# Kernel optimization log

Hardware: AMD Instinct MI355X
Metric: run time of the kernel (lower is better)

## Reference

```python
import jax, jax.numpy as jnp
import numpy as np

RC, RMIN = 6.0, 0.5
BETA, M1, M2 = 12, 24, 6
B, N, NT, MN = 4, 1024, 2, 128
K = NT * MN
NFEAT = M1 * M2


def _cheby(x, order):
    # Chebyshev polynomials T_0..T_{order-1} via recurrence, stacked on last axis
    Ts = [jnp.ones_like(x), x]
    for _ in range(order - 2):
        Ts.append(2.0 * x * Ts[-1] - Ts[-2])
    return jnp.stack(Ts[:order], axis=-1)


def _feat_fn(rxyz, valid, ti_map, c_param, scale):
    # rxyz: (B,N,K,3) neighbor displacement vectors; valid: (B,N,K) 0/1 float
    b, n, k, _ = rxyz.shape
    r = jnp.sqrt(jnp.sum(rxyz * rxyz, axis=-1) + 1e-12)          # (B,N,K)
    u = jnp.clip((r - RMIN) / (RC - RMIN), 0.0, 1.0)
    fc = 0.5 * (jnp.cos(jnp.pi * u) + 1.0) * valid                # smooth cutoff
    x = 2.0 * (r - RMIN) / (RC - RMIN) - 1.0
    T = _cheby(x, BETA).reshape(b, n, NT, MN, BETA)               # group slots by neighbor type
    c_i = c_param[ti_map]                                         # (N, NT, M1, BETA) gather by center type
    s = jnp.einsum('bntmk,ntfk->bntmf', T, c_i).reshape(b, n, k, M1)
    s = s * fc[..., None]                                         # (B,N,K,M1)
    inv_r = valid / r
    sr = jnp.concatenate([valid[..., None], rxyz * inv_r[..., None]], axis=-1)  # (B,N,K,4)
    R = jnp.einsum('bnkf,bnkc->bnfc', s, sr) / MN                 # (B,N,M1,4)
    feat = jnp.einsum('bnfc,bngc->bnfg', R, R[:, :, :M2]).reshape(b, n, NFEAT)
    return feat * scale


def _ei_fn(feat, ti_map, W0, b0, W1, b1, W2, b2, ener_shift):
    # evaluate all per-type fitting nets, then select by atom type
    h = jnp.tanh(jnp.einsum('bnf,tfh->bnth', feat, W0) + b0)
    h2 = jnp.tanh(jnp.einsum('bnth,thg->bntg', h, W1) + b1) + h   # resnet skip
    E = jnp.einsum('bnth,th->bnt', h2, W2) + b2 + ener_shift      # (B,N,T)
    idx = jnp.broadcast_to(ti_map[None, :, None], (E.shape[0], E.shape[1], 1))
    return jnp.take_along_axis(E, idx, axis=2)[..., 0]            # (B,N)


def setup_inputs() -> dict:
    key = jax.random.key(0)
    ks = jax.random.split(key, 16)
    num_neigh = jax.random.randint(ks[0], (B, N, NT), MN // 2, MN + 1)
    slot = jnp.arange(MN)
    vmask = slot[None, None, None, :] < num_neigh[..., None]      # (B,N,NT,MN)
    ln = jax.random.randint(ks[1], (B, N, NT, MN), 0, N)
    list_neigh = jnp.where(vmask, ln, -1)
    r = jax.random.uniform(ks[2], (B, N, K), minval=RMIN + 0.2, maxval=RC - 0.1)
    d = jax.random.normal(ks[3], (B, N, K, 3))
    d = d / jnp.linalg.norm(d, axis=-1, keepdims=True)
    rxyz = d * r[..., None]
    vm = vmask.reshape(B, N, K).astype(jnp.float32)
    ImageDR = jnp.concatenate([r[..., None], rxyz], axis=-1) * vm[..., None]
    return {
        'list_neigh': list_neigh,
        'Imagetype_map': jax.random.randint(ks[4], (N,), 0, NT),
        'atom_type': jnp.arange(NT),
        'ImageDR': ImageDR.astype(jnp.float32),
        'num_neigh': num_neigh,
        'nghost': 0,
        'c_param': jax.random.normal(ks[5], (NT, NT, M1, BETA), jnp.float32) * 0.3,
        'scale': jax.random.uniform(ks[6], (NFEAT,), jnp.float32, 0.5, 1.5),
        'W0': jax.random.normal(ks[7], (NT, NFEAT, 128), jnp.float32) * 0.08,
        'b0': jnp.zeros((NT, 128), jnp.float32),
        'W1': jax.random.normal(ks[8], (NT, 128, 128), jnp.float32) * 0.08,
        'b1': jnp.zeros((NT, 128), jnp.float32),
        'W2': jax.random.normal(ks[9], (NT, 128), jnp.float32) * 0.08,
        'b2': jnp.zeros((NT,), jnp.float32),
        'ener_shift': jax.random.normal(ks[10], (NT,), jnp.float32),
    }


def reference(list_neigh, Imagetype_map, atom_type, ImageDR, num_neigh, nghost,
              c_param, scale, W0, b0, W1, b1, W2, b2, ener_shift):
    ln = list_neigh.reshape(B, N, K)
    valid = (ln >= 0).astype(ImageDR.dtype)
    rxyz = ImageDR[..., 1:4]

    def etot(z):
        feat = _feat_fn(z, valid, Imagetype_map, c_param, scale)
        return _ei_fn(feat, Imagetype_map, W0, b0, W1, b1, W2, b2, ener_shift)

    Ei = etot(rxyz)                                               # (B,N)
    Etot = jnp.sum(Ei, axis=1)                                    # (B,)
    g = jax.grad(lambda z: etot(z).sum())(rxyz)                   # dE/dr_ij  (B,N,K,3)

    natom_tot = N + nghost
    Force = jnp.zeros((B, natom_tot, 3), ImageDR.dtype)
    Force = Force.at[:, :N].add(g.sum(axis=2))                    # center-atom contribution
    idx = jnp.where(ln >= 0, ln, natom_tot).reshape(B, N * K)     # invalid -> pad slot

    def scat(i, v):
        buf = jnp.zeros((natom_tot + 1, 3), v.dtype)
        return buf.at[i].add(v)[:natom_tot]

    Force = Force + jax.vmap(scat)(idx, (-g).reshape(B, N * K, 3))  # scatter to neighbors
    Virial = -jnp.einsum('bnkc,bnkd->bcd', rxyz, g).reshape(B, 9)
    return (Etot, Ei, Force, Virial)
```

## Files before the change

### kernel.cpp

```cpp
#include <hip/hip_runtime.h>
#include <math.h>

#define RMINF  0.5f
#define LSPAN  5.5f
constexpr int BETA = 12, M1 = 24, M2 = 6;
constexpr int B_ = 4, N_ = 1024, NT_ = 2, MN_ = 128;
constexpr int K_ = NT_ * MN_;
constexpr int NFEAT = M1 * M2;
constexpr int HID = 128;
constexpr float PI_F = 3.14159265358979323846f;

constexpr int EI_OFF = B_;
constexpr int F_OFF  = B_ + B_ * N_;
constexpr int V_OFF  = F_OFF + B_ * N_ * 3;

constexpr int G_ = 4;
constexpr int NG = B_ * N_ / G_;
constexpr int SL = 8;

constexpr size_t WS_FEAT    = 0;
constexpr size_t WS_R       = (size_t)B_ * N_ * NFEAT;
constexpr size_t WS_VIR     = WS_R + (size_t)B_ * N_ * 96;
constexpr size_t WS_CONTRIB = WS_VIR + (size_t)NG * 9;
constexpr size_t WS_PARTIAL = WS_CONTRIB + (size_t)NG * N_ * 3;


__global__ __launch_bounds__(256) void k1_embed(
    const int*   __restrict__ list_neigh,
    const int*   __restrict__ type_map,
    const float* __restrict__ imagedr,
    const float* __restrict__ c_param,
    const float* __restrict__ scale,
    float* __restrict__ feat_ws,
    float* __restrict__ R_ws)
{
    __shared__ float c_sh[NT_ * M1 * BETA];
    __shared__ float p_sh[K_][13];
    __shared__ float sr_sh[K_][5];
    __shared__ float Mpart[2][96];
    __shared__ float R_sh[96];

    const int tid = threadIdx.x;
    const int bn = blockIdx.x;
    const int n  = bn % N_;
    const int tn = type_map[n];

    for (int i = tid; i < NT_ * M1 * BETA; i += 256)
        c_sh[i] = c_param[tn * (NT_ * M1 * BETA) + i];

    const int k = tid;
    const int lni = list_neigh[(size_t)bn * K_ + k];
    const float valid = (lni >= 0) ? 1.0f : 0.0f;

    const float4 dr4 = reinterpret_cast<const float4*>(imagedr)[(size_t)bn * K_ + k];
    const float rx = dr4.y, ry = dr4.z, rz = dr4.w;
    const float r  = sqrtf(rx*rx + ry*ry + rz*rz + 1e-12f);
    const float uraw = (r - RMINF) / LSPAN;
    const float u  = fminf(fmaxf(uraw, 0.0f), 1.0f);
    const float fc = 0.5f * (cosf(PI_F * u) + 1.0f) * valid;
    const float x  = 2.0f * (r - RMINF) / LSPAN - 1.0f;

    float T[BETA];
    T[0] = 1.0f; T[1] = x;
#pragma unroll
    for (int j = 2; j < BETA; ++j) T[j] = 2.0f * x * T[j-1] - T[j-2];

    const float inv_r = 1.0f / r;
    sr_sh[k][0] = valid;
    sr_sh[k][1] = valid * rx * inv_r;
    sr_sh[k][2] = valid * ry * inv_r;
    sr_sh[k][3] = valid * rz * inv_r;
#pragma unroll
    for (int j = 0; j < BETA; ++j) p_sh[k][j] = fc * T[j];
    __syncthreads();

    if (tid < 192) {
        const int sub = tid / 96, idx = tid % 96;
        const int tk = idx / 48, rem = idx % 48;
        const int j = rem >> 2, cc = rem & 3;
        const int k0 = tk * 128 + sub * 64;
        float a0 = 0.0f, a1 = 0.0f;
        for (int kk = k0; kk < k0 + 64; kk += 2) {
            a0 = fmaf(p_sh[kk][j],   sr_sh[kk][cc],   a0);
            a1 = fmaf(p_sh[kk+1][j], sr_sh[kk+1][cc], a1);
        }
        Mpart[sub][idx] = a0 + a1;
    }
    __syncthreads();

    if (tid < 96) {
        const int f = tid >> 2, cc = tid & 3;
        float acc = 0.0f;
#pragma unroll
        for (int tk = 0; tk < NT_; ++tk) {
#pragma unroll
            for (int j = 0; j < BETA; ++j) {
                const float m = Mpart[0][tk*48 + j*4 + cc] + Mpart[1][tk*48 + j*4 + cc];
                acc = fmaf(c_sh[tk*288 + f*12 + j], m, acc);
            }
        }
        const float v = acc * (1.0f / MN_);
        R_sh[tid] = v;
        R_ws[(size_t)bn * 96 + tid] = v;
    }
    __syncthreads();
    if (tid < NFEAT) {
        const int f = tid / 6, g = tid % 6;
        float acc = 0.0f;
#pragma unroll
        for (int c = 0; c < 4; ++c) acc += R_sh[f * 4 + c] * R_sh[g * 4 + c];
        feat_ws[(size_t)bn * NFEAT + tid] = acc * scale[tid];
    }
}

__global__ __launch_bounds__(512) void k2_mlp(
    const int*   __restrict__ type_map,
    const float* __restrict__ scale,
    const float* __restrict__ W0,
    const float* __restrict__ b0,
    const float* __restrict__ W1,
    const float* __restrict__ b1,
    const float* __restrict__ W2,
    const float* __restrict__ b2,
    const float* __restrict__ eshift,
    const float* __restrict__ feat_ws,
    float* __restrict__ dfeat_ws,
    float* __restrict__ out)
{
    __shared__ float feat_sh[4][NFEAT];
    __shared__ float h_sh[4][HID];
    __shared__ float dz1_sh[4][HID];
    __shared__ float dz0_sh[4][HID];
    __shared__ float red[8];

    const int tid  = threadIdx.x;
    const int b    = tid >> 7;
    const int c    = tid & 127;
    const int lane = tid & 63;
    const int wid  = tid >> 6;
    const int n  = blockIdx.x;
    const int tn = type_map[n];

    for (int i = tid; i < 4 * NFEAT; i += 512) {
        const int bb = i / NFEAT, f = i % NFEAT;
        feat_sh[bb][f] = feat_ws[((size_t)bb * N_ + n) * NFEAT + f];
    }
    __syncthreads();

    float acc = b0[tn * HID + c];
    const float* w0c = W0 + (size_t)tn * NFEAT * HID + c;
#pragma unroll 8
    for (int f = 0; f < NFEAT; ++f)
        acc = fmaf(feat_sh[b][f], w0c[(size_t)f * HID], acc);
    const float h = tanhf(acc);
    h_sh[b][c] = h;
    __syncthreads();

    float acc1 = b1[tn * HID + c];
    const float* w1c = W1 + (size_t)tn * HID * HID + c;
#pragma unroll 8
    for (int g = 0; g < HID; ++g)
        acc1 = fmaf(h_sh[b][g], w1c[(size_t)g * HID], acc1);
    const float t1 = tanhf(acc1);
    const float w2c = W2[tn * HID + c];
    dz1_sh[b][c] = w2c * (1.0f - t1 * t1);

    {
        float v = (t1 + h) * w2c;
#pragma unroll
        for (int m = 32; m >= 1; m >>= 1) v += __shfl_xor(v, m);
        if (lane == 0) red[wid] = v;
    }
    __syncthreads();
    if (tid < 4)
        out[EI_OFF + (size_t)tid * N_ + n] =
            red[tid * 2] + red[tid * 2 + 1] + b2[tn] + eshift[tn];

    {
        const float4* w1row = reinterpret_cast<const float4*>(W1 + (size_t)(tn * HID + c) * HID);
        float ar = w2c, arb = 0.0f;
#pragma unroll 4
        for (int g4 = 0; g4 < HID / 4; g4 += 2) {
            const float4 w  = w1row[g4];
            const float4 w2 = w1row[g4 + 1];
            ar  += w.x  * dz1_sh[b][g4*4+0] + w.y  * dz1_sh[b][g4*4+1]
                 + w.z  * dz1_sh[b][g4*4+2] + w.w  * dz1_sh[b][g4*4+3];
            arb += w2.x * dz1_sh[b][g4*4+4] + w2.y * dz1_sh[b][g4*4+5]
                 + w2.z * dz1_sh[b][g4*4+6] + w2.w * dz1_sh[b][g4*4+7];
        }
        dz0_sh[b][c] = (ar + arb) * (1.0f - h * h);
    }
    __syncthreads();

    for (int f = c; f < NFEAT; f += HID) {
        const float4* w0row = reinterpret_cast<const float4*>(W0 + (size_t)(tn * NFEAT + f) * HID);
        float ar = 0.0f, arb = 0.0f;
#pragma unroll 4
        for (int h4 = 0; h4 < HID / 4; h4 += 2) {
            const float4 w  = w0row[h4];
            const float4 w2 = w0row[h4 + 1];
            ar  += w.x  * dz0_sh[b][h4*4+0] + w.y  * dz0_sh[b][h4*4+1]
                 + w.z  * dz0_sh[b][h4*4+2] + w.w  * dz0_sh[b][h4*4+3];
            arb += w2.x * dz0_sh[b][h4*4+4] + w2.y * dz0_sh[b][h4*4+5]
                 + w2.z * dz0_sh[b][h4*4+6] + w2.w * dz0_sh[b][h4*4+7];
        }
        dfeat_ws[((size_t)b * N_ + n) * NFEAT + f] = (ar + arb) * scale[f];
    }
}

__global__ __launch_bounds__(256) void k3_bwd(
    const int*   __restrict__ list_neigh,
    const int*   __restrict__ type_map,
    const float* __restrict__ imagedr,
    const float* __restrict__ c_param,
    const float* __restrict__ dfeat_ws,
    const float* __restrict__ R_ws,
    float* __restrict__ contrib_ws,
    float* __restrict__ vir_ws)
{
    __shared__ float fcontrib[N_ * 3];
    __shared__ float c_sh[NT_ * M1 * BETA];
    __shared__ float dfeat_sh[NFEAT];
    __shared__ float R_sh[96];
    __shared__ float dR_sh[96];
    __shared__ float A_sh[96];
    __shared__ float red12[12 * 4];

    const int tid  = threadIdx.x;
    const int lane = tid & 63;
    const int wid  = tid >> 6;
    const int g  = blockIdx.x;
    const int tk = tid >> 7;

    for (int i = tid; i < N_ * 3; i += 256) fcontrib[i] = 0.0f;

    float vv0=0.f,vv1=0.f,vv2=0.f,vv3=0.f,vv4=0.f,vv5=0.f,vv6=0.f,vv7=0.f,vv8=0.f;

    for (int aa = 0; aa < G_; ++aa) {
        const int bn = g * G_ + aa;
        const int n  = bn & (N_ - 1);
        const int tn = type_map[n];

        __syncthreads();
        for (int i = tid; i < NT_ * M1 * BETA; i += 256)
            c_sh[i] = c_param[tn * (NT_ * M1 * BETA) + i];
        if (tid < NFEAT) dfeat_sh[tid] = dfeat_ws[(size_t)bn * NFEAT + tid];
        if (tid < 96)    R_sh[tid]     = R_ws[(size_t)bn * 96 + tid];
        __syncthreads();

        if (tid < 96) {
            const int p = tid >> 2, c = tid & 3;
            float acc = 0.0f;
#pragma unroll
            for (int gg = 0; gg < M2; ++gg) acc += dfeat_sh[p * 6 + gg] * R_sh[gg * 4 + c];
            if (p < M2) {
                for (int f = 0; f < M1; ++f) acc += dfeat_sh[f * 6 + p] * R_sh[f * 4 + c];
            }
            dR_sh[p * 4 + c] = acc * (1.0f / MN_);
        }
        __syncthreads();

        if (tid < 96) {
            const int atk = tid / 48, rem = tid % 48;
            const int j = rem >> 2, cc = rem & 3;
            float acc = 0.0f;
#pragma unroll
            for (int f = 0; f < M1; ++f)
                acc = fmaf(c_sh[atk*288 + f*12 + j], dR_sh[f*4 + cc], acc);
            A_sh[tid] = acc;
        }
        __syncthreads();

        const int lni = list_neigh[(size_t)bn * K_ + tid];
        const float valid = (lni >= 0) ? 1.0f : 0.0f;
        const float4 dr4 = reinterpret_cast<const float4*>(imagedr)[(size_t)bn * K_ + tid];
        const float rx = dr4.y, ry = dr4.z, rz = dr4.w;
        const float r  = sqrtf(rx*rx + ry*ry + rz*rz + 1e-12f);
        const float uraw = (r - RMINF) / LSPAN;
        const float u  = fminf(fmaxf(uraw, 0.0f), 1.0f);
        const float fc = 0.5f * (cosf(PI_F * u) + 1.0f) * valid;
        const float x  = 2.0f * (r - RMINF) / LSPAN - 1.0f;

        float T[BETA];
        T[0] = 1.0f; T[1] = x;
#pragma unroll
        for (int j = 2; j < BETA; ++j) T[j] = 2.0f * x * T[j-1] - T[j-2];

        const float inv_r = 1.0f / r;
        const float sr0 = valid;
        const float sr1 = valid * rx * inv_r;
        const float sr2 = valid * ry * inv_r;
        const float sr3 = valid * rz * inv_r;

        const float* Arow = &A_sh[tk * 48];
        float dfc = 0.0f, dx = 0.0f;
        float tA0 = 0.0f, tA1 = 0.0f, tA2 = 0.0f, tA3 = 0.0f;
        float tpm1 = 1.0f, tpm2 = 0.0f;
#pragma unroll
        for (int j = 0; j < BETA; ++j) {
            const float a0 = Arow[j*4+0], a1 = Arow[j*4+1];
            const float a2 = Arow[j*4+2], a3 = Arow[j*4+3];
            const float cjj = a0*sr0 + a1*sr1 + a2*sr2 + a3*sr3;
            dfc = fmaf(T[j], cjj, dfc);
            tA0 = fmaf(T[j], a0, tA0);
            tA1 = fmaf(T[j], a1, tA1);
            tA2 = fmaf(T[j], a2, tA2);
            tA3 = fmaf(T[j], a3, tA3);
            if (j == 1) {
                dx = cjj;
            } else if (j >= 2) {
                const float tp = 2.0f * T[j-1] + 2.0f * x * tpm1 - tpm2;
                dx = fmaf(cjj, tp, dx);
                tpm2 = tpm1; tpm1 = tp;
            }
        }
        const float dsr1 = fc * tA1, dsr2 = fc * tA2, dsr3 = fc * tA3;

        float dfcdr = 0.0f;
        if (uraw > 0.0f && uraw < 1.0f)
            dfcdr = -0.5f * PI_F * sinf(PI_F * u) * valid / LSPAN;
        const float drt = (fc * dx) * (2.0f / LSPAN) + dfc * dfcdr;
        const float Sdot = dsr1 * rx + dsr2 * ry + dsr3 * rz;
        const float common = drt * inv_r - valid * Sdot * inv_r * inv_r * inv_r;
        const float gx = common * rx + valid * dsr1 * inv_r;
        const float gy = common * ry + valid * dsr2 * inv_r;
        const float gz = common * rz + valid * dsr3 * inv_r;

        if (lni >= 0) {
            atomicAdd(&fcontrib[lni * 3 + 0], -gx);
            atomicAdd(&fcontrib[lni * 3 + 1], -gy);
            atomicAdd(&fcontrib[lni * 3 + 2], -gz);
        }

        {
            float s0 = gx, s1 = gy, s2 = gz;
#pragma unroll
            for (int m = 32; m >= 1; m >>= 1) {
                s0 += __shfl_xor(s0, m);
                s1 += __shfl_xor(s1, m);
                s2 += __shfl_xor(s2, m);
            }
            if (lane == 0) {
                red12[0 * 4 + wid] = s0;
                red12[1 * 4 + wid] = s1;
                red12[2 * 4 + wid] = s2;
            }
        }
        __syncthreads();
        if (tid < 3) {
            const float v = red12[tid*4+0] + red12[tid*4+1] + red12[tid*4+2] + red12[tid*4+3];
            atomicAdd(&fcontrib[n * 3 + tid], v);
        }

        vv0 = fmaf(-rx, gx, vv0); vv1 = fmaf(-rx, gy, vv1); vv2 = fmaf(-rx, gz, vv2);
        vv3 = fmaf(-ry, gx, vv3); vv4 = fmaf(-ry, gy, vv4); vv5 = fmaf(-ry, gz, vv5);
        vv6 = fmaf(-rz, gx, vv6); vv7 = fmaf(-rz, gy, vv7); vv8 = fmaf(-rz, gz, vv8);
    }

    {
        float vals[9] = {vv0,vv1,vv2,vv3,vv4,vv5,vv6,vv7,vv8};
        __syncthreads();
#pragma unroll
        for (int i = 0; i < 9; ++i) {
            float v = vals[i];
#pragma unroll
            for (int m = 32; m >= 1; m >>= 1) v += __shfl_xor(v, m);
            if (lane == 0) red12[i * 4 + wid] = v;
        }
        __syncthreads();
        if (tid < 9)
            vir_ws[(size_t)g * 9 + tid] = red12[tid*4+0] + red12[tid*4+1]
                                        + red12[tid*4+2] + red12[tid*4+3];
    }

    __syncthreads();
    {
        float4* dst = reinterpret_cast<float4*>(contrib_ws + (size_t)g * (N_ * 3));
        const float4* src = reinterpret_cast<const float4*>(fcontrib);
        for (int i = tid; i < (N_ * 3) / 4; i += 256) dst[i] = src[i];
    }
}

__global__ __launch_bounds__(256) void k3_reduce(
    const float* __restrict__ contrib_ws,
    float* __restrict__ partial_ws)
{
    const int x  = blockIdx.x;
    const int ch = x % 3;
    const int bb = (x / 3) % B_;
    const int s  = x / (3 * B_);
    const int c4 = ch * 256 + threadIdx.x;
    const int rows = (NG / B_) / SL;
    const int g0 = bb * (NG / B_) + s * rows;

    const float4* src = reinterpret_cast<const float4*>(contrib_ws);
    float4 a0 = {0,0,0,0}, a1 = {0,0,0,0};
    for (int r = 0; r < rows; r += 2) {
        const float4 v0 = src[(size_t)(g0 + r)     * 768 + c4];
        const float4 v1 = src[(size_t)(g0 + r + 1) * 768 + c4];
        a0.x += v0.x; a0.y += v0.y; a0.z += v0.z; a0.w += v0.w;
        a1.x += v1.x; a1.y += v1.y; a1.z += v1.z; a1.w += v1.w;
    }
    const float4 res = {a0.x + a1.x, a0.y + a1.y, a0.z + a1.z, a0.w + a1.w};
    reinterpret_cast<float4*>(partial_ws)[(size_t)(s * B_ + bb) * 768 + c4] = res;
}

__global__ __launch_bounds__(256) void k4_final(
    const float* __restrict__ vir_ws,
    const float* __restrict__ partial_ws,
    float* __restrict__ out)
{
    __shared__ float red[10 * 4];
    const int tid  = threadIdx.x;
    const int lane = tid & 63;
    const int wid  = tid >> 6;
    const int b = blockIdx.x;

    for (int i = tid; i < N_ * 3; i += 256) {
        float f = 0.0f;
#pragma unroll
        for (int s = 0; s < SL; ++s) f += partial_ws[(size_t)(s * B_ + b) * (N_ * 3) + i];
        out[F_OFF + (size_t)b * (N_ * 3) + i] = f;
    }

    float vals[10];
#pragma unroll
    for (int i = 0; i < 10; ++i) vals[i] = 0.0f;
    for (int n = tid; n < N_; n += 256) vals[0] += out[EI_OFF + b * N_ + n];
    {
        const float* vp = vir_ws + ((size_t)b * (NG / B_) + tid) * 9;
#pragma unroll
        for (int j = 0; j < 9; ++j) vals[1 + j] = vp[j];
    }
#pragma unroll
    for (int i = 0; i < 10; ++i) {
        float v = vals[i];
#pragma unroll
        for (int m = 32; m >= 1; m >>= 1) v += __shfl_xor(v, m);
        if (lane == 0) red[i * 4 + wid] = v;
    }
    __syncthreads();
    if (tid < 10) {
        const float v = red[tid*4+0] + red[tid*4+1] + red[tid*4+2] + red[tid*4+3];
        if (tid == 0) out[b] = v;
        else          out[V_OFF + b * 9 + (tid - 1)] = v;
    }
}

extern "C" void kernel_launch(void* const* d_in, const int* in_sizes, int n_in,
                              void* d_out, int out_size, void* d_ws, size_t ws_size,
                              hipStream_t stream) {
    float* out = (float*)d_out;
    float* ws  = (float*)d_ws;
    float* feat_ws    = ws + WS_FEAT;
    float* R_ws       = ws + WS_R;
    float* vir_ws     = ws + WS_VIR;
    float* contrib_ws = ws + WS_CONTRIB;
    float* partial_ws = ws + WS_PARTIAL;

    const int*   list_neigh = (const int*)d_in[0];
    const int*   type_map   = (const int*)d_in[1];
    const float* imagedr    = (const float*)d_in[3];
    const float* c_param    = (const float*)d_in[6];
    const float* scale      = (const float*)d_in[7];
    const float* W0 = (const float*)d_in[8];
    const float* b0 = (const float*)d_in[9];
    const float* W1 = (const float*)d_in[10];
    const float* b1 = (const float*)d_in[11];
    const float* W2 = (const float*)d_in[12];
    const float* b2 = (const float*)d_in[13];
    const float* eshift = (const float*)d_in[14];

    k1_embed<<<B_ * N_, 256, 0, stream>>>(list_neigh, type_map, imagedr, c_param,
                                          scale, feat_ws, R_ws);
    k2_mlp<<<N_, 512, 0, stream>>>(type_map, scale, W0, b0, W1, b1, W2, b2,
                                   eshift, feat_ws, feat_ws , out);
    k3_bwd<<<NG, 256, 0, stream>>>(list_neigh, type_map, imagedr, c_param,
                                   feat_ws , R_ws, contrib_ws, vir_ws);
    k3_reduce<<<SL * B_ * 3, 256, 0, stream>>>(contrib_ws, partial_ws);
    k4_final<<<B_, 256, 0, stream>>>(vir_ws, partial_ws, out);
}
```

Baseline: 234.6 us.

## Restructure MLP kernel to stage weight tiles in LDS and reuse across batches

The per-atom MLP kernel now launches 128 threads instead of 512, and each thread computes all four batch entries for one hidden unit. Weights are staged in padded LDS chunks of 32 rows, so each weight element is read once from global memory and reused for all four batches. The backward passes load transposed tiles into LDS instead of doing strided row reads. In exchange, blocks run fewer threads and add many more barriers, which reduces parallelism per block.

```diff
diff --git a/kernel.cpp b/kernel.cpp
--- a/kernel.cpp
+++ b/kernel.cpp
@@ -113,7 +113,7 @@
     }
 }
 
-__global__ __launch_bounds__(512) void k2_mlp(
+__global__ __launch_bounds__(128) void k2_mlp(
     const int*   __restrict__ type_map,
     const float* __restrict__ scale,
     const float* __restrict__ W0,
@@ -127,84 +127,148 @@
     float* __restrict__ dfeat_ws,
     float* __restrict__ out)
 {
+    constexpr int WS = 145;
     __shared__ float feat_sh[4][NFEAT];
     __shared__ float h_sh[4][HID];
     __shared__ float dz1_sh[4][HID];
     __shared__ float dz0_sh[4][HID];
-    __shared__ float red[8];
+    __shared__ float wbuf[32 * WS];
+    __shared__ float red2[4][2];
 
     const int tid  = threadIdx.x;
-    const int b    = tid >> 7;
-    const int c    = tid & 127;
+    const int c    = tid;
     const int lane = tid & 63;
-    const int wid  = tid >> 6;
+    const int wv   = tid >> 6;
     const int n  = blockIdx.x;
     const int tn = type_map[n];
 
-    for (int i = tid; i < 4 * NFEAT; i += 512) {
+    for (int i = tid; i < 4 * NFEAT; i += 128) {
         const int bb = i / NFEAT, f = i % NFEAT;
         feat_sh[bb][f] = feat_ws[((size_t)bb * N_ + n) * NFEAT + f];
     }
-    __syncthreads();
-
-    float acc = b0[tn * HID + c];
-    const float* w0c = W0 + (size_t)tn * NFEAT * HID + c;
-#pragma unroll 8
-    for (int f = 0; f < NFEAT; ++f)
-        acc = fmaf(feat_sh[b][f], w0c[(size_t)f * HID], acc);
-    const float h = tanhf(acc);
-    h_sh[b][c] = h;
-    __syncthreads();
-
-    float acc1 = b1[tn * HID + c];
-    const float* w1c = W1 + (size_t)tn * HID * HID + c;
-#pragma unroll 8
-    for (int g = 0; g < HID; ++g)
-        acc1 = fmaf(h_sh[b][g], w1c[(size_t)g * HID], acc1);
-    const float t1 = tanhf(acc1);
+
+    const float* W0t = W0 + (size_t)tn * NFEAT * HID;
+    const float* W1t = W1 + (size_t)tn * HID * HID;
+
+    float acc[4];
+    {
+        const float bias = b0[tn * HID + c];
+        acc[0] = acc[1] = acc[2] = acc[3] = bias;
+    }
+    for (int ch = 0; ch < NFEAT; ch += 32) {
+        const int rows = (NFEAT - ch) < 32 ? (NFEAT - ch) : 32;
+        __syncthreads();
+        for (int i = tid; i < rows * 128; i += 128) {
+            const int f = i >> 7, cc = i & 127;
+            wbuf[f * WS + cc] = W0t[(size_t)(ch + f) * HID + cc];
+        }
+        __syncthreads();
+#pragma unroll 4
+        for (int f = 0; f < rows; ++f) {
+            const float w = wbuf[f * WS + c];
+#pragma unroll
+            for (int b = 0; b < 4; ++b)
+                acc[b] = fmaf(feat_sh[b][ch + f], w, acc[b]);
+        }
+    }
+    float hv[4];
+#pragma unroll
+    for (int b = 0; b < 4; ++b) { hv[b] = tanhf(acc[b]); h_sh[b][c] = hv[b]; }
+
+    {
+        const float bias = b1[tn * HID + c];
+        acc[0] = acc[1] = acc[2] = acc[3] = bias;
+    }
+    for (int ch = 0; ch < HID; ch += 32) {
+        __syncthreads();
+        for (int i = tid; i < 32 * 128; i += 128) {
+            const int g = i >> 7, cc = i & 127;
+            wbuf[g * WS + cc] = W1t[(size_t)(ch + g) * HID + cc];
+        }
+        __syncthreads();
+#pragma unroll 4
+        for (int g = 0; g < 32; ++g) {
+            const float w = wbuf[g * WS + c];
+#pragma unroll
+            for (int b = 0; b < 4; ++b)
+                acc[b] = fmaf(h_sh[b][ch + g], w, acc[b]);
+        }
+    }
+
     const float w2c = W2[tn * HID + c];
-    dz1_sh[b][c] = w2c * (1.0f - t1 * t1);
-
-    {
-        float v = (t1 + h) * w2c;
+    float ei[4];
+#pragma unroll
+    for (int b = 0; b < 4; ++b) {
+        const float t1 = tanhf(acc[b]);
+        dz1_sh[b][c] = w2c * (1.0f - t1 * t1);
+        ei[b] = (t1 + hv[b]) * w2c;
+    }
+#pragma unroll
+    for (int b = 0; b < 4; ++b) {
+        float v = ei[b];
 #pragma unroll
         for (int m = 32; m >= 1; m >>= 1) v += __shfl_xor(v, m);
-        if (lane == 0) red[wid] = v;
+        if (lane == 0) red2[b][wv] = v;
     }
     __syncthreads();
     if (tid < 4)
         out[EI_OFF + (size_t)tid * N_ + n] =
-            red[tid * 2] + red[tid * 2 + 1] + b2[tn] + eshift[tn];
-
+            red2[tid][0] + red2[tid][1] + b2[tn] + eshift[tn];
+
+    acc[0] = acc[1] = acc[2] = acc[3] = w2c;
+    for (int ch = 0; ch < HID; ch += 32) {
+        __syncthreads();
+        for (int i = tid; i < 32 * 128; i += 128) {
+            const int j = i & 31, hh = i >> 5;
+            wbuf[j * WS + hh] = W1t[(size_t)hh * HID + ch + j];
+        }
+        __syncthreads();
+#pragma unroll 4
+        for (int j = 0; j < 32; ++j) {
+            const float w = wbuf[j * WS + c];
+#pragma unroll
+            for (int b = 0; b < 4; ++b)
+                acc[b] = fmaf(dz1_sh[b][ch + j], w, acc[b]);
+        }
+    }
+#pragma unroll
+    for (int b = 0; b < 4; ++b) dz0_sh[b][c] = acc[b] * (1.0f - hv[b] * hv[b]);
+
+    float d0[4] = {0.f, 0.f, 0.f, 0.f};
+    float d1[4] = {0.f, 0.f, 0.f, 0.f};
+    for (int ch = 0; ch < HID; ch += 32) {
+        __syncthreads();
+        for (int i = tid; i < 32 * NFEAT; i += 128) {
+            const int j = i & 31, f = i >> 5;
+            wbuf[j * WS + f] = W0t[(size_t)f * HID + ch + j];
+        }
+        __syncthreads();
+#pragma unroll 4
+        for (int j = 0; j < 32; ++j) {
+            const float w = wbuf[j * WS + c];
+            float z[4];
+#pragma unroll
+            for (int b = 0; b < 4; ++b) z[b] = dz0_sh[b][ch + j];
+#pragma unroll
+            for (int b = 0; b < 4; ++b) d0[b] = fmaf(w, z[b], d0[b]);
+            if (c < NFEAT - HID) {
+                const float w2 = wbuf[j * WS + HID + c];
+#pragma unroll
+                for (int b = 0; b < 4; ++b) d1[b] = fmaf(w2, z[b], d1[b]);
+            }
+        }
+    }
     {
-        const float4* w1row = reinterpret_cast<const float4*>(W1 + (size_t)(tn * HID + c) * HID);
-        float ar = w2c, arb = 0.0f;
-#pragma unroll 4
-        for (int g4 = 0; g4 < HID / 4; g4 += 2) {
-            const float4 w  = w1row[g4];
-            const float4 w2 = w1row[g4 + 1];
-            ar  += w.x  * dz1_sh[b][g4*4+0] + w.y  * dz1_sh[b][g4*4+1]
-                 + w.z  * dz1_sh[b][g4*4+2] + w.w  * dz1_sh[b][g4*4+3];
-            arb += w2.x * dz1_sh[b][g4*4+4] + w2.y * dz1_sh[b][g4*4+5]
-                 + w2.z * dz1_sh[b][g4*4+6] + w2.w * dz1_sh[b][g4*4+7];
-        }
-        dz0_sh[b][c] = (ar + arb) * (1.0f - h * h);
-    }
-    __syncthreads();
-
-    for (int f = c; f < NFEAT; f += HID) {
-        const float4* w0row = reinterpret_cast<const float4*>(W0 + (size_t)(tn * NFEAT + f) * HID);
-        float ar = 0.0f, arb = 0.0f;
-#pragma unroll 4
-        for (int h4 = 0; h4 < HID / 4; h4 += 2) {
-            const float4 w  = w0row[h4];
-            const float4 w2 = w0row[h4 + 1];
-            ar  += w.x  * dz0_sh[b][h4*4+0] + w.y  * dz0_sh[b][h4*4+1]
-                 + w.z  * dz0_sh[b][h4*4+2] + w.w  * dz0_sh[b][h4*4+3];
-            arb += w2.x * dz0_sh[b][h4*4+4] + w2.y * dz0_sh[b][h4*4+5]
-                 + w2.z * dz0_sh[b][h4*4+6] + w2.w * dz0_sh[b][h4*4+7];
-        }
-        dfeat_ws[((size_t)b * N_ + n) * NFEAT + f] = (ar + arb) * scale[f];
+        const float sc = scale[c];
+#pragma unroll
+        for (int b = 0; b < 4; ++b)
+            dfeat_ws[((size_t)b * N_ + n) * NFEAT + c] = d0[b] * sc;
+        if (c < NFEAT - HID) {
+            const float sc2 = scale[HID + c];
+#pragma unroll
+            for (int b = 0; b < 4; ++b)
+                dfeat_ws[((size_t)b * N_ + n) * NFEAT + HID + c] = d1[b] * sc2;
+        }
     }
 }
 
@@ -473,7 +537,7 @@
 
     k1_embed<<<B_ * N_, 256, 0, stream>>>(list_neigh, type_map, imagedr, c_param,
                                           scale, feat_ws, R_ws);
-    k2_mlp<<<N_, 512, 0, stream>>>(type_map, scale, W0, b0, W1, b1, W2, b2,
+    k2_mlp<<<N_, 128, 0, stream>>>(type_map, scale, W0, b0, W1, b1, W2, b2,
                                    eshift, feat_ws, feat_ws , out);
     k3_bwd<<<NG, 256, 0, stream>>>(list_neigh, type_map, imagedr, c_param,
                                    feat_ws , R_ws, contrib_ws, vir_ws);
```

Result: faster. 207.6 us (-11.5%).
